# Kernel optimization log

Measured on AMD Instinct MI355X. Metric: run time of the kernel, lower is better.

Reference implementation:

```python
import jax, jax.numpy as jnp
import numpy as np

N = 100000      # nodes
E = 1600000     # edges (avg degree 16)
F_N, F_E, H = 5, 3, 64
L = 3           # num GCN layers


def setup_inputs() -> dict:
    key = jax.random.key(0)
    ks = jax.random.split(key, 20)
    s = 0.05
    p = lambda k, shape: jax.random.normal(k, shape, jnp.float32) * s
    return {
        "x": jax.random.normal(ks[0], (N, F_N), jnp.float32),
        "edge_index": jax.random.randint(ks[1], (2, E), 0, N, dtype=jnp.int32),
        "edge_attr": jax.random.normal(ks[2], (E, F_E), jnp.float32),
        # node / edge encoders
        "Wn": p(ks[3], (F_N, H)), "bn": jnp.zeros((H,), jnp.float32),
        "We": p(ks[4], (F_E, H)), "be": jnp.zeros((H,), jnp.float32),
        # stacked GCNConv weights [L, H, H] and biases [L, H]
        "Wc": p(ks[5], (L, H, H)), "bc": jnp.zeros((L, H), jnp.float32),
        # demand forecast head
        "Wd1": p(ks[6], (H, H // 2)), "bd1": jnp.zeros((H // 2,), jnp.float32),
        "Wd2": p(ks[7], (H // 2, 1)), "bd2": jnp.zeros((1,), jnp.float32),
        # inventory optimizer head
        "Wi1": p(ks[8], (H, H // 2)), "bi1": jnp.zeros((H // 2,), jnp.float32),
        "Wi2": p(ks[9], (H // 2, 1)), "bi2": jnp.zeros((1,), jnp.float32),
    }


def reference(x, edge_index, edge_attr, Wn, bn, We, be, Wc, bc,
              Wd1, bd1, Wd2, bd2, Wi1, bi1, Wi2, bi2):
    src, dst = edge_index[0], edge_index[1]
    n = x.shape[0]

    h = jax.nn.relu(x @ Wn + bn)                      # [N, H]
    _ea = jax.nn.relu(edge_attr @ We + be)            # encoded edge feats (GCNConv ignores them)

    # GCN symmetric normalization with self-loops: deg[i] = in_degree(i) + 1
    ones_e = jnp.ones(src.shape[0], h.dtype)
    deg = jax.ops.segment_sum(ones_e, dst, num_segments=n) + 1.0
    dinv = jax.lax.rsqrt(deg)                         # [N]
    norm_e = dinv[src] * dinv[dst]                    # [E]
    norm_self = (dinv * dinv)[:, None]                # [N, 1]

    for l in range(Wc.shape[0]):
        hw = h @ Wc[l]                                # [N, H]
        msgs = norm_e[:, None] * hw[src]              # gather + scale, [E, H]
        agg = jax.ops.segment_sum(msgs, dst, num_segments=n) + norm_self * hw
        h = jax.nn.relu(agg + bc[l])

    demand = jax.nn.relu(h @ Wd1 + bd1) @ Wd2 + bd2   # [N, 1]
    inventory = jax.nn.relu(h @ Wi1 + bi1) @ Wi2 + bi2
    return demand, inventory
```

## Files before the change

kernel.cpp:

```cpp
#include <hip/hip_runtime.h>

#define H 64
#define FN 5
#define EPB 4096
#define BSHIFT 8
#define CAP2 4864

typedef _Float16 half4 __attribute__((ext_vector_type(4)));
typedef _Float16 half8 __attribute__((ext_vector_type(8)));
typedef float    float8v __attribute__((ext_vector_type(8)));

__global__ void k_bscatter2(const int* __restrict__ src, const int* __restrict__ dst,
                            int* __restrict__ lofs_t, int* __restrict__ bcounts,
                            int* __restrict__ binned, int nE, int nbB, int nbE) {
    __shared__ int lh[512], lpos[512], lcur[512], tmp[256];
    __shared__ int stage[EPB];
    int t = threadIdx.x;
    int e0 = blockIdx.x * EPB;
    int es[16], ed[16];
    lh[t] = 0; lh[t + 256] = 0;
    __syncthreads();
#pragma unroll
    for (int i = 0; i < 16; ++i) {
        int e = e0 + i * 256 + t;
        bool v = e < nE;
        es[i] = v ? src[e] : 0;
        ed[i] = v ? dst[e] : -1;
        if (v) atomicAdd(&lh[ed[i] >> BSHIFT], 1);
    }
    __syncthreads();
    int a0 = lh[2 * t], a1 = lh[2 * t + 1];
    tmp[t] = a0 + a1;
    __syncthreads();
    for (int s = 1; s < 256; s <<= 1) {
        int a = (t >= s) ? tmp[t - s] : 0;
        __syncthreads();
        tmp[t] += a;
        __syncthreads();
    }
    int ex = tmp[t] - (a0 + a1);
    lpos[2 * t] = ex;
    lpos[2 * t + 1] = ex + a0;
    __syncthreads();
    lcur[t] = lpos[t]; lcur[t + 256] = lpos[t + 256];
    for (int b = t; b <= nbB; b += 256) lofs_t[(size_t)b * nbE + blockIdx.x] = lpos[b];
    for (int b = t; b < nbB; b += 256) if (lh[b]) atomicAdd(&bcounts[b], lh[b]);
    __syncthreads();
#pragma unroll
    for (int i = 0; i < 16; ++i) {
        if (ed[i] >= 0) {
            int b = ed[i] >> BSHIFT;
            int p = atomicAdd(&lcur[b], 1);
            stage[p] = es[i] | ((ed[i] & 255) << 17);
        }
    }
    __syncthreads();
    int total = lpos[nbB];
    for (int j = t; j < total; j += 256) binned[e0 + j] = stage[j];
}

__global__ void k_bcsr2(const int* __restrict__ binned, const int* __restrict__ lofs_t,
                        const int* __restrict__ bcounts, int* __restrict__ row_ptr,
                        int* __restrict__ csr_src, float* __restrict__ dinv,
                        const float* __restrict__ x, const float* __restrict__ Wn,
                        const float* __restrict__ bn, _Float16* __restrict__ g0,
                        int n, int nE, int nbE, int nbB) {
    __shared__ int start_s[512], roff[513], tmp[256];
    __shared__ int deg[256], st[256], cur[256];
    __shared__ int lbuf[CAP2];
    __shared__ int stage2[CAP2];
    int t = threadIdx.x;
    int B = blockIdx.x;
    int node0 = B << BSHIFT;
    int nn = min(256, n - node0);

    {
        int v0 = (t < B) ? bcounts[t] : 0;
        int v1 = (t + 256 < B) ? bcounts[t + 256] : 0;
        tmp[t] = v0 + v1;
    }
    __syncthreads();
    for (int s = 1; s < 256; s <<= 1) {
        int a = (t >= s) ? tmp[t - s] : 0;
        __syncthreads();
        tmp[t] += a;
        __syncthreads();
    }
    int base = tmp[255];
    __syncthreads();

    int s0i = 2 * t, s1i = 2 * t + 1;
    int a0 = 0, a1 = 0;
    if (s0i < nbE) {
        int o0 = lofs_t[B * nbE + s0i], o1 = lofs_t[(B + 1) * nbE + s0i];
        a0 = o1 - o0;
        start_s[s0i] = s0i * EPB + o0;
    } else start_s[s0i] = 0;
    if (s1i < nbE) {
        int o0 = lofs_t[B * nbE + s1i], o1 = lofs_t[(B + 1) * nbE + s1i];
        a1 = o1 - o0;
        start_s[s1i] = s1i * EPB + o0;
    } else start_s[s1i] = 0;
    tmp[t] = a0 + a1;
    __syncthreads();
    for (int s = 1; s < 256; s <<= 1) {
        int a = (t >= s) ? tmp[t - s] : 0;
        __syncthreads();
        tmp[t] += a;
        __syncthreads();
    }
    int ex = tmp[t] - (a0 + a1);
    roff[2 * t] = ex;
    roff[2 * t + 1] = ex + a0;
    if (t == 255) roff[512] = tmp[255];
    __syncthreads();
    int total = min(roff[512], CAP2);
    for (int i = t; i < total; i += 256) {
        int lo = 0, hi = 512;
        while (hi - lo > 1) {
            int mid = (lo + hi) >> 1;
            if (roff[mid] <= i) lo = mid; else hi = mid;
        }
        lbuf[i] = binned[start_s[lo] + (i - roff[lo])];
    }
    deg[t] = 0;
    __syncthreads();
    for (int i = t; i < total; i += 256) atomicAdd(&deg[(lbuf[i] >> 17) & 255], 1);
    __syncthreads();
    tmp[t] = deg[t];
    __syncthreads();
    for (int s = 1; s < 256; s <<= 1) {
        int a = (t >= s) ? tmp[t - s] : 0;
        __syncthreads();
        tmp[t] += a;
        __syncthreads();
    }
    st[t] = tmp[t] - deg[t];
    cur[t] = st[t];
    __syncthreads();
    float dvv = 1.0f / sqrtf((float)deg[t] + 1.0f);
    if (t < nn) {
        row_ptr[node0 + t] = base + st[t];
        dinv[node0 + t] = dvv;
    }
    if (B == 0 && t == 0) row_ptr[n] = nE;
    for (int i = t; i < total; i += 256) {
        int p0 = lbuf[i];
        int p = atomicAdd(&cur[(p0 >> 17) & 255], 1);
        int sv = p0 & 0x1FFFF;
        if (p < CAP2) stage2[p] = sv;
        else csr_src[base + p] = sv;
    }
    __syncthreads();
    for (int i = t; i < total; i += 256) csr_src[base + i] = stage2[i];

    if (t < nn) {
        int node = node0 + t;
        float xr[FN];
#pragma unroll
        for (int k = 0; k < FN; ++k) xr[k] = x[(size_t)node * FN + k];
#pragma unroll
        for (int c0 = 0; c0 < H; c0 += 8) {
            half8 hh;
#pragma unroll
            for (int j = 0; j < 8; ++j) {
                float acc = bn[c0 + j];
#pragma unroll
                for (int k = 0; k < FN; ++k)
                    acc += xr[k] * Wn[k * H + c0 + j];
                hh[j] = (_Float16)(fmaxf(acc, 0.f) * dvv);
            }
            *(half8*)(g0 + (size_t)node * H + c0) = hh;
        }
    }
}

__global__ void k_layer(const _Float16* __restrict__ gin, const int* __restrict__ csr_src,
                        const int* __restrict__ row_ptr, const float* __restrict__ dinv,
                        const float* __restrict__ W, const float* __restrict__ bias,
                        _Float16* __restrict__ gout, float* __restrict__ hout,
                        int n, int last) {
    __shared__ float As[64 * 68];
    __shared__ int rp_s[65];
    __shared__ float dv_s[64];
    int t = threadIdx.x;
    int wave = t >> 6, lane = t & 63;
    int base = blockIdx.x * 64;
    if (t < 65) rp_s[t] = row_ptr[min(base + t, n)];
    if (t >= 128 && t < 192) {
        int nd = base + (t - 128);
        dv_s[t - 128] = (nd < n) ? dinv[nd] : 0.f;
    }
    __syncthreads();

    int c8 = (lane >> 3) * 8;
    int slot = lane & 7;
    for (int it = 0; it < 8; ++it) {
        int rA = it * 8 + wave, rB = rA + 4;
        int nodeA = base + rA, nodeB = base + rB;
        float8v accA = 0.f, accB = 0.f;
        int iA = rp_s[rA], eA = rp_s[rA + 1];
        int iB = rp_s[rB], eB = rp_s[rB + 1];
        int cA = (eA - iA) >> 3, cB = (eB - iB) >> 3;
        int xA = 0, xB = 0, txA = 0, txB = 0;
        int tbA = iA + (cA << 3), tbB = iB + (cB << 3);
        bool tvA = (tbA + slot < eA), tvB = (tbB + slot < eB);
        if (cA) xA = csr_src[iA + slot];
        if (cB) xB = csr_src[iB + slot];
        if (tvA) txA = csr_src[tbA + slot];
        if (tvB) txB = csr_src[tbB + slot];
        while (cA && cB) {
            half8 vA = *(const half8*)(gin + (size_t)xA * H + c8);
            half8 vB = *(const half8*)(gin + (size_t)xB * H + c8);
            iA += 8; iB += 8; --cA; --cB;
            if (cA) xA = csr_src[iA + slot];
            if (cB) xB = csr_src[iB + slot];
#pragma unroll
            for (int k = 0; k < 8; ++k) { accA[k] += (float)vA[k]; accB[k] += (float)vB[k]; }
        }
        while (cA) {
            half8 vA = *(const half8*)(gin + (size_t)xA * H + c8);
            iA += 8; --cA;
            if (cA) xA = csr_src[iA + slot];
#pragma unroll
            for (int k = 0; k < 8; ++k) accA[k] += (float)vA[k];
        }
        while (cB) {
            half8 vB = *(const half8*)(gin + (size_t)xB * H + c8);
            iB += 8; --cB;
            if (cB) xB = csr_src[iB + slot];
#pragma unroll
            for (int k = 0; k < 8; ++k) accB[k] += (float)vB[k];
        }
        if (tvA) {
            half8 vA = *(const half8*)(gin + (size_t)txA * H + c8);
#pragma unroll
            for (int k = 0; k < 8; ++k) accA[k] += (float)vA[k];
        }
        if (tvB) {
            half8 vB = *(const half8*)(gin + (size_t)txB * H + c8);
#pragma unroll
            for (int k = 0; k < 8; ++k) accB[k] += (float)vB[k];
        }
#pragma unroll
        for (int m = 1; m <= 4; m <<= 1) {
#pragma unroll
            for (int k = 0; k < 8; ++k) {
                accA[k] += __shfl_xor(accA[k], m, 64);
                accB[k] += __shfl_xor(accB[k], m, 64);
            }
        }
        if (slot == 0) {
            float oA[8], oB[8];
            if (nodeA < n) {
                half8 sA = *(const half8*)(gin + (size_t)nodeA * H + c8);
                float dA = dv_s[rA];
#pragma unroll
                for (int k = 0; k < 8; ++k) oA[k] = (accA[k] + (float)sA[k]) * dA;
            } else {
#pragma unroll
                for (int k = 0; k < 8; ++k) oA[k] = 0.f;
            }
            if (nodeB < n) {
                half8 sB = *(const half8*)(gin + (size_t)nodeB * H + c8);
                float dB = dv_s[rB];
#pragma unroll
                for (int k = 0; k < 8; ++k) oB[k] = (accB[k] + (float)sB[k]) * dB;
            } else {
#pragma unroll
                for (int k = 0; k < 8; ++k) oB[k] = 0.f;
            }
            *(float4*)&As[rA * 68 + c8]     = make_float4(oA[0], oA[1], oA[2], oA[3]);
            *(float4*)&As[rA * 68 + c8 + 4] = make_float4(oA[4], oA[5], oA[6], oA[7]);
            *(float4*)&As[rB * 68 + c8]     = make_float4(oB[0], oB[1], oB[2], oB[3]);
            *(float4*)&As[rB * 68 + c8 + 4] = make_float4(oB[4], oB[5], oB[6], oB[7]);
        }
    }
    __syncthreads();

    int tx = t & 15, ty = t >> 4;
    int c0 = tx * 4;
    const float* a0 = As + (ty * 4 + 0) * 68;
    const float* a1 = As + (ty * 4 + 1) * 68;
    const float* a2 = As + (ty * 4 + 2) * 68;
    const float* a3 = As + (ty * 4 + 3) * 68;
    float4 acc0 = make_float4(0.f, 0.f, 0.f, 0.f);
    float4 acc1 = acc0, acc2 = acc0, acc3 = acc0;
#pragma unroll 16
    for (int k = 0; k < H; ++k) {
        float4 w = *(const float4*)(W + k * H + c0);
        float v0 = a0[k], v1 = a1[k], v2 = a2[k], v3 = a3[k];
        acc0.x += v0 * w.x; acc0.y += v0 * w.y; acc0.z += v0 * w.z; acc0.w += v0 * w.w;
        acc1.x += v1 * w.x; acc1.y += v1 * w.y; acc1.z += v1 * w.z; acc1.w += v1 * w.w;
        acc2.x += v2 * w.x; acc2.y += v2 * w.y; acc2.z += v2 * w.z; acc2.w += v2 * w.w;
        acc3.x += v3 * w.x; acc3.y += v3 * w.y; acc3.z += v3 * w.z; acc3.w += v3 * w.w;
    }
    float4 b = *(const float4*)(bias + c0);
    float4 accs[4] = {acc0, acc1, acc2, acc3};
#pragma unroll
    for (int rr = 0; rr < 4; ++rr) {
        int r = ty * 4 + rr;
        int row = base + r;
        if (row < n) {
            float4 o;
            o.x = fmaxf(accs[rr].x + b.x, 0.f);
            o.y = fmaxf(accs[rr].y + b.y, 0.f);
            o.z = fmaxf(accs[rr].z + b.z, 0.f);
            o.w = fmaxf(accs[rr].w + b.w, 0.f);
            if (last) {
                *(float4*)(hout + (size_t)row * H + c0) = o;
            } else {
                float d = dv_s[r];
                half4 hh;
                hh.x = (_Float16)(o.x * d);
                hh.y = (_Float16)(o.y * d);
                hh.z = (_Float16)(o.z * d);
                hh.w = (_Float16)(o.w * d);
                *(half4*)(gout + (size_t)row * H + c0) = hh;
            }
        }
    }
}

__global__ void k_heads(const float* __restrict__ h,
                        const float* __restrict__ Wd1, const float* __restrict__ bd1,
                        const float* __restrict__ Wd2, const float* __restrict__ bd2,
                        const float* __restrict__ Wi1, const float* __restrict__ bi1,
                        const float* __restrict__ Wi2, const float* __restrict__ bi2,
                        float* __restrict__ out, int n) {
    __shared__ float hs[64 * 65];
    int lane = threadIdx.x;
    int base = blockIdx.x * 64;
    for (int r = 0; r < 64; ++r) {
        int row = base + r;
        hs[r * 65 + lane] = (row < n) ? h[(size_t)row * H + lane] : 0.f;
    }
    __syncthreads();

    float accd[32], acci[32];
#pragma unroll
    for (int j = 0; j < 32; ++j) { accd[j] = bd1[j]; acci[j] = bi1[j]; }
    for (int k = 0; k < H; ++k) {
        float hk = hs[lane * 65 + k];
#pragma unroll
        for (int j = 0; j < 32; ++j) {
            accd[j] += hk * Wd1[k * 32 + j];
            acci[j] += hk * Wi1[k * 32 + j];
        }
    }
    float demand = bd2[0], inventory = bi2[0];
#pragma unroll
    for (int j = 0; j < 32; ++j) {
        demand    += fmaxf(accd[j], 0.f) * Wd2[j];
        inventory += fmaxf(acci[j], 0.f) * Wi2[j];
    }
    int node = base + lane;
    if (node < n) {
        out[node] = demand;
        out[n + node] = inventory;
    }
}

extern "C" void kernel_launch(void* const* d_in, const int* in_sizes, int n_in,
                              void* d_out, int out_size, void* d_ws, size_t ws_size,
                              hipStream_t stream) {
    const float* x   = (const float*)d_in[0];
    const int*   ei  = (const int*)  d_in[1];
    const float* Wn  = (const float*)d_in[3];
    const float* bn  = (const float*)d_in[4];
    const float* Wc  = (const float*)d_in[7];
    const float* bc  = (const float*)d_in[8];
    const float* Wd1 = (const float*)d_in[9];
    const float* bd1 = (const float*)d_in[10];
    const float* Wd2 = (const float*)d_in[11];
    const float* bd2 = (const float*)d_in[12];
    const float* Wi1 = (const float*)d_in[13];
    const float* bi1 = (const float*)d_in[14];
    const float* Wi2 = (const float*)d_in[15];
    const float* bi2 = (const float*)d_in[16];

    const int n  = in_sizes[0] / FN;
    const int nE = in_sizes[1] / 2;
    const int* src = ei;
    const int* dst = ei + nE;

    const int nbE = (nE + EPB - 1) / EPB;
    const int nbB = (n + 255) >> BSHIFT;
    const int nbL = (n + 63) / 64;

    char* w = (char*)d_ws;
#define CARVE(TYPE, NAME, BYTES) \
    TYPE* NAME = (TYPE*)w; w += (((size_t)(BYTES)) + 255) & ~(size_t)255;
    CARVE(int,      binned,  (size_t)nbE * EPB * 4)
    CARVE(int,      csr_src, (size_t)nE * 4)
    CARVE(int,      row_ptr, (size_t)(n + 4) * 4)
    CARVE(float,    dinv,    (size_t)n * 4)
    CARVE(int,      lofs,    (size_t)(nbB + 1) * nbE * 4)
    CARVE(int,      bcounts, 512 * 4)
    CARVE(float,    hbuf,    (size_t)n * H * 4)
    CARVE(_Float16, gA,      (size_t)n * H * 2)
    CARVE(_Float16, gB,      (size_t)n * H * 2)
#undef CARVE

    hipMemsetAsync(bcounts, 0, 512 * 4, stream);

    k_bscatter2<<<nbE, 256, 0, stream>>>(src, dst, lofs, bcounts, binned, nE, nbB, nbE);
    k_bcsr2    <<<nbB, 256, 0, stream>>>(binned, lofs, bcounts, row_ptr, csr_src,
                                         dinv, x, Wn, bn, gA, n, nE, nbE, nbB);

    k_layer<<<nbL, 256, 0, stream>>>(gA, csr_src, row_ptr, dinv, Wc,
                                     bc, gB, hbuf, n, 0);
    k_layer<<<nbL, 256, 0, stream>>>(gB, csr_src, row_ptr, dinv, Wc + (size_t)H * H,
                                     bc + H, gA, hbuf, n, 0);
    k_layer<<<nbL, 256, 0, stream>>>(gA, csr_src, row_ptr, dinv, Wc + (size_t)2 * H * H,
                                     bc + 2 * H, gB, hbuf, n, 1);

    k_heads<<<(n + 63) / 64, 64, 0, stream>>>(hbuf, Wd1, bd1, Wd2, bd2,
                                              Wi1, bi1, Wi2, bi2, (float*)d_out, n);
}
```

Before: 368.9 us.

## Replace two-pass binned CSR build with global-atomic degree count and fill

Replaces the block-binned scatter and per-bucket local CSR construction with three simpler kernels. One computes per-node in-degree with global atomics, one scans degrees into row pointers and cursors while also encoding nodes, and one scatters src indices into CSR slots via global atomicAdd on per-node cursors. This drops the staging buffer, the lofs table and the binary-search gather. In exchange it adds a launch, heavy global atomic contention on 1.6M edges, and a nondeterministic neighbor order within each row, which can change float summation order and locality in the layer kernels.

```diff
diff --git a/kernel.cpp b/kernel.cpp
--- a/kernel.cpp
+++ b/kernel.cpp
@@ -4,33 +4,48 @@
 #define FN 5
 #define EPB 4096
 #define BSHIFT 8
-#define CAP2 4864
 
 typedef _Float16 half4 __attribute__((ext_vector_type(4)));
 typedef _Float16 half8 __attribute__((ext_vector_type(8)));
 typedef float    float8v __attribute__((ext_vector_type(8)));
 
-__global__ void k_bscatter2(const int* __restrict__ src, const int* __restrict__ dst,
-                            int* __restrict__ lofs_t, int* __restrict__ bcounts,
-                            int* __restrict__ binned, int nE, int nbB, int nbE) {
-    __shared__ int lh[512], lpos[512], lcur[512], tmp[256];
-    __shared__ int stage[EPB];
+__global__ void k_deg(const int* __restrict__ dst, int* __restrict__ deg,
+                      int* __restrict__ bcounts, int nE, int nbB) {
+    __shared__ int lh[512];
     int t = threadIdx.x;
     int e0 = blockIdx.x * EPB;
-    int es[16], ed[16];
     lh[t] = 0; lh[t + 256] = 0;
     __syncthreads();
 #pragma unroll
     for (int i = 0; i < 16; ++i) {
         int e = e0 + i * 256 + t;
-        bool v = e < nE;
-        es[i] = v ? src[e] : 0;
-        ed[i] = v ? dst[e] : -1;
-        if (v) atomicAdd(&lh[ed[i] >> BSHIFT], 1);
-    }
-    __syncthreads();
-    int a0 = lh[2 * t], a1 = lh[2 * t + 1];
-    tmp[t] = a0 + a1;
+        if (e < nE) {
+            int d = dst[e];
+            atomicAdd(&deg[d], 1);
+            atomicAdd(&lh[d >> BSHIFT], 1);
+        }
+    }
+    __syncthreads();
+    for (int b = t; b < nbB; b += 256) if (lh[b]) atomicAdd(&bcounts[b], lh[b]);
+}
+
+__global__ void k_rowptr_enc(const int* __restrict__ bcounts, const int* __restrict__ deg,
+                             int* __restrict__ row_ptr, int* __restrict__ cur,
+                             float* __restrict__ dinv,
+                             const float* __restrict__ x, const float* __restrict__ Wn,
+                             const float* __restrict__ bn, _Float16* __restrict__ g0,
+                             int n, int nE, int nbB) {
+    __shared__ int tmp[256];
+    int t = threadIdx.x;
+    int B = blockIdx.x;
+    int node0 = B << BSHIFT;
+    int nn = min(256, n - node0);
+
+    {
+        int v0 = (t < B) ? bcounts[t] : 0;
+        int v1 = (t + 256 < B) ? bcounts[t + 256] : 0;
+        tmp[t] = v0 + v1;
+    }
     __syncthreads();
     for (int s = 1; s < 256; s <<= 1) {
         int a = (t >= s) ? tmp[t - s] : 0;
@@ -38,47 +53,11 @@
         tmp[t] += a;
         __syncthreads();
     }
-    int ex = tmp[t] - (a0 + a1);
-    lpos[2 * t] = ex;
-    lpos[2 * t + 1] = ex + a0;
-    __syncthreads();
-    lcur[t] = lpos[t]; lcur[t + 256] = lpos[t + 256];
-    for (int b = t; b <= nbB; b += 256) lofs_t[(size_t)b * nbE + blockIdx.x] = lpos[b];
-    for (int b = t; b < nbB; b += 256) if (lh[b]) atomicAdd(&bcounts[b], lh[b]);
-    __syncthreads();
-#pragma unroll
-    for (int i = 0; i < 16; ++i) {
-        if (ed[i] >= 0) {
-            int b = ed[i] >> BSHIFT;
-            int p = atomicAdd(&lcur[b], 1);
-            stage[p] = es[i] | ((ed[i] & 255) << 17);
-        }
-    }
-    __syncthreads();
-    int total = lpos[nbB];
-    for (int j = t; j < total; j += 256) binned[e0 + j] = stage[j];
-}
-
-__global__ void k_bcsr2(const int* __restrict__ binned, const int* __restrict__ lofs_t,
-                        const int* __restrict__ bcounts, int* __restrict__ row_ptr,
-                        int* __restrict__ csr_src, float* __restrict__ dinv,
-                        const float* __restrict__ x, const float* __restrict__ Wn,
-                        const float* __restrict__ bn, _Float16* __restrict__ g0,
-                        int n, int nE, int nbE, int nbB) {
-    __shared__ int start_s[512], roff[513], tmp[256];
-    __shared__ int deg[256], st[256], cur[256];
-    __shared__ int lbuf[CAP2];
-    __shared__ int stage2[CAP2];
-    int t = threadIdx.x;
-    int B = blockIdx.x;
-    int node0 = B << BSHIFT;
-    int nn = min(256, n - node0);
-
-    {
-        int v0 = (t < B) ? bcounts[t] : 0;
-        int v1 = (t + 256 < B) ? bcounts[t + 256] : 0;
-        tmp[t] = v0 + v1;
-    }
+    int base = tmp[255];
+    __syncthreads();
+
+    int d = (t < nn) ? deg[node0 + t] : 0;
+    tmp[t] = d;
     __syncthreads();
     for (int s = 1; s < 256; s <<= 1) {
         int a = (t >= s) ? tmp[t - s] : 0;
@@ -86,73 +65,15 @@
         tmp[t] += a;
         __syncthreads();
     }
-    int base = tmp[255];
-    __syncthreads();
-
-    int s0i = 2 * t, s1i = 2 * t + 1;
-    int a0 = 0, a1 = 0;
-    if (s0i < nbE) {
-        int o0 = lofs_t[B * nbE + s0i], o1 = lofs_t[(B + 1) * nbE + s0i];
-        a0 = o1 - o0;
-        start_s[s0i] = s0i * EPB + o0;
-    } else start_s[s0i] = 0;
-    if (s1i < nbE) {
-        int o0 = lofs_t[B * nbE + s1i], o1 = lofs_t[(B + 1) * nbE + s1i];
-        a1 = o1 - o0;
-        start_s[s1i] = s1i * EPB + o0;
-    } else start_s[s1i] = 0;
-    tmp[t] = a0 + a1;
-    __syncthreads();
-    for (int s = 1; s < 256; s <<= 1) {
-        int a = (t >= s) ? tmp[t - s] : 0;
-        __syncthreads();
-        tmp[t] += a;
-        __syncthreads();
-    }
-    int ex = tmp[t] - (a0 + a1);
-    roff[2 * t] = ex;
-    roff[2 * t + 1] = ex + a0;
-    if (t == 255) roff[512] = tmp[255];
-    __syncthreads();
-    int total = min(roff[512], CAP2);
-    for (int i = t; i < total; i += 256) {
-        int lo = 0, hi = 512;
-        while (hi - lo > 1) {
-            int mid = (lo + hi) >> 1;
-            if (roff[mid] <= i) lo = mid; else hi = mid;
-        }
-        lbuf[i] = binned[start_s[lo] + (i - roff[lo])];
-    }
-    deg[t] = 0;
-    __syncthreads();
-    for (int i = t; i < total; i += 256) atomicAdd(&deg[(lbuf[i] >> 17) & 255], 1);
-    __syncthreads();
-    tmp[t] = deg[t];
-    __syncthreads();
-    for (int s = 1; s < 256; s <<= 1) {
-        int a = (t >= s) ? tmp[t - s] : 0;
-        __syncthreads();
-        tmp[t] += a;
-        __syncthreads();
-    }
-    st[t] = tmp[t] - deg[t];
-    cur[t] = st[t];
-    __syncthreads();
-    float dvv = 1.0f / sqrtf((float)deg[t] + 1.0f);
+    int st = tmp[t] - d;
+    float dvv = 1.0f / sqrtf((float)d + 1.0f);
     if (t < nn) {
-        row_ptr[node0 + t] = base + st[t];
+        int rp = base + st;
+        row_ptr[node0 + t] = rp;
+        cur[node0 + t] = rp;
         dinv[node0 + t] = dvv;
     }
     if (B == 0 && t == 0) row_ptr[n] = nE;
-    for (int i = t; i < total; i += 256) {
-        int p0 = lbuf[i];
-        int p = atomicAdd(&cur[(p0 >> 17) & 255], 1);
-        int sv = p0 & 0x1FFFF;
-        if (p < CAP2) stage2[p] = sv;
-        else csr_src[base + p] = sv;
-    }
-    __syncthreads();
-    for (int i = t; i < total; i += 256) csr_src[base + i] = stage2[i];
 
     if (t < nn) {
         int node = node0 + t;
@@ -171,6 +92,20 @@
                 hh[j] = (_Float16)(fmaxf(acc, 0.f) * dvv);
             }
             *(half8*)(g0 + (size_t)node * H + c0) = hh;
+        }
+    }
+}
+
+__global__ void k_fill(const int* __restrict__ src, const int* __restrict__ dst,
+                       int* __restrict__ cur, int* __restrict__ csr_src, int nE) {
+    int t = threadIdx.x;
+    int e0 = blockIdx.x * EPB;
+#pragma unroll
+    for (int i = 0; i < 16; ++i) {
+        int e = e0 + i * 256 + t;
+        if (e < nE) {
+            int p = atomicAdd(&cur[dst[e]], 1);
+            csr_src[p] = src[e];
         }
     }
 }
@@ -391,22 +326,24 @@
     char* w = (char*)d_ws;
 #define CARVE(TYPE, NAME, BYTES) \
     TYPE* NAME = (TYPE*)w; w += (((size_t)(BYTES)) + 255) & ~(size_t)255;
-    CARVE(int,      binned,  (size_t)nbE * EPB * 4)
     CARVE(int,      csr_src, (size_t)nE * 4)
     CARVE(int,      row_ptr, (size_t)(n + 4) * 4)
+    CARVE(int,      deg,     (size_t)n * 4)
+    CARVE(int,      cur,     (size_t)n * 4)
     CARVE(float,    dinv,    (size_t)n * 4)
-    CARVE(int,      lofs,    (size_t)(nbB + 1) * nbE * 4)
     CARVE(int,      bcounts, 512 * 4)
     CARVE(float,    hbuf,    (size_t)n * H * 4)
     CARVE(_Float16, gA,      (size_t)n * H * 2)
     CARVE(_Float16, gB,      (size_t)n * H * 2)
 #undef CARVE
 
+    hipMemsetAsync(deg, 0, (size_t)n * 4, stream);
     hipMemsetAsync(bcounts, 0, 512 * 4, stream);
 
-    k_bscatter2<<<nbE, 256, 0, stream>>>(src, dst, lofs, bcounts, binned, nE, nbB, nbE);
-    k_bcsr2    <<<nbB, 256, 0, stream>>>(binned, lofs, bcounts, row_ptr, csr_src,
-                                         dinv, x, Wn, bn, gA, n, nE, nbE, nbB);
+    k_deg       <<<nbE, 256, 0, stream>>>(dst, deg, bcounts, nE, nbB);
+    k_rowptr_enc<<<nbB, 256, 0, stream>>>(bcounts, deg, row_ptr, cur, dinv,
+                                          x, Wn, bn, gA, n, nE, nbB);
+    k_fill      <<<nbE, 256, 0, stream>>>(src, dst, cur, csr_src, nE);
 
     k_layer<<<nbL, 256, 0, stream>>>(gA, csr_src, row_ptr, dinv, Wc,
                                      bc, gB, hbuf, n, 0);
```

Result: slower. 528.2 us (+43.2%).
